# Optimization experiments

Measured on AMD Instinct MI355X. Metric: run time of the kernel, lower is better.

## Reference

```python
import jax, jax.numpy as jnp
import numpy as np

N = 100000
E = 3200000
NEG_SLOPE = 0.2  # PyG GATConv default


def gat_layer(x, src, dst, W, a_src, a_dst, b, heads, out_ch, concat):
    # per-node linear transform, split into heads: [N, H, C]
    h = (x @ W).reshape(N, heads, out_ch)
    # per-node attention logits: [N, H]
    al_src = jnp.sum(h * a_src, axis=-1)
    al_dst = jnp.sum(h * a_dst, axis=-1)
    # per-edge attention coefficient (x_j = source, x_i = target): [E, H]
    e = jax.nn.leaky_relu(al_src[src] + al_dst[dst], NEG_SLOPE)
    # segment softmax over incoming edges of each destination node
    m = jax.ops.segment_max(e, dst, num_segments=N)
    e = jnp.exp(e - m[dst])
    denom = jax.ops.segment_sum(e, dst, num_segments=N)
    alpha = e / (denom[dst] + 1e-16)
    # weighted message aggregation: scatter-add over dst
    msg = h[src] * alpha[..., None]  # [E, H, C]
    out = jax.ops.segment_sum(msg, dst, num_segments=N)  # [N, H, C]
    out = out.reshape(N, heads * out_ch) if concat else out.mean(axis=1)
    return out + b


def setup_inputs() -> dict:
    key = jax.random.key(0)
    ks = jax.random.split(key, 11)
    return {
        "x": jax.random.normal(ks[0], (N, 2), dtype=jnp.float32),
        "edge_index": jax.random.randint(ks[1], (2, E), 0, N, dtype=jnp.int64),
        "edge_attr": jax.random.normal(ks[2], (E, 1), dtype=jnp.float32),
        "W1": jax.random.normal(ks[3], (2, 32), dtype=jnp.float32) * 0.5,
        "att_src1": jax.random.normal(ks[4], (4, 8), dtype=jnp.float32) * 0.3,
        "att_dst1": jax.random.normal(ks[5], (4, 8), dtype=jnp.float32) * 0.3,
        "b1": jnp.zeros((32,), dtype=jnp.float32),
        "W2": jax.random.normal(ks[6], (32, 2), dtype=jnp.float32) * 0.2,
        "att_src2": jax.random.normal(ks[7], (1, 2), dtype=jnp.float32) * 0.3,
        "att_dst2": jax.random.normal(ks[8], (1, 2), dtype=jnp.float32) * 0.3,
        "b2": jnp.zeros((2,), dtype=jnp.float32),
    }


def reference(x, edge_index, edge_attr, W1, att_src1, att_dst1, b1, W2, att_src2, att_dst2, b2):
    # add self-loops (PyG GATConv default add_self_loops=True)
    loops = jnp.arange(N, dtype=edge_index.dtype)
    src = jnp.concatenate([edge_index[0], loops])
    dst = jnp.concatenate([edge_index[1], loops])
    h = gat_layer(x, src, dst, W1, att_src1, att_dst1, b1, heads=4, out_ch=8, concat=True)
    h = jax.nn.elu(h)
    out = gat_layer(h, src, dst, W2, att_src2, att_dst2, b2, heads=1, out_ch=2, concat=False)
    return out
```

## Files before the change

kernel.cpp:

```cpp
#include <hip/hip_runtime.h>
#include <math.h>

#define NEG_SLOPE 0.2f
#define BK_BITS 9
#define BK (1 << BK_BITS)
#define SBITS 17
#define SMASK ((1 << SBITS) - 1)
#define CAP 20480
#define PPT2 20
#define SW(p) ((p) ^ (((p) >> 5) & 31))

__device__ __forceinline__ float lrelu(float x) { return x > 0.f ? x : NEG_SLOPE * x; }

__global__ void init_bcur(int* __restrict__ bcur, int NB) {
    int i = threadIdx.x;
    if (i < NB) bcur[i] = i * CAP;
}

__global__ __launch_bounds__(256) void bucket_scatter(const int* __restrict__ src,
                                                      const int* __restrict__ dst,
                                                      int* __restrict__ bcur,
                                                      int* __restrict__ pairs, int E) {
    __shared__ int cnt[256], sc[256], off[256], cur[256], gbase[256];
    __shared__ int lpair[4096];
    __shared__ unsigned char lbkt[4096];
    int t = threadIdx.x;
    cnt[t] = 0;
    __syncthreads();

    int E4 = E >> 2;
    const int4* src4 = (const int4*)src;
    const int4* dst4 = (const int4*)dst;
    int base4 = blockIdx.x * 1024;
    int4 d4[4], s4[4];
    bool val[4];
#pragma unroll
    for (int k = 0; k < 4; k++) {
        int i4 = base4 + k * 256 + t;
        val[k] = (i4 < E4);
        if (val[k]) {
            d4[k] = dst4[i4];
            s4[k] = src4[i4];
            atomicAdd(&cnt[d4[k].x >> BK_BITS], 1);
            atomicAdd(&cnt[d4[k].y >> BK_BITS], 1);
            atomicAdd(&cnt[d4[k].z >> BK_BITS], 1);
            atomicAdd(&cnt[d4[k].w >> BK_BITS], 1);
        }
    }
    int dt = -1, st = 0;
    if (blockIdx.x == gridDim.x - 1) {
        int e = (E4 << 2) + t;
        if (e < E) { dt = dst[e]; st = src[e]; atomicAdd(&cnt[dt >> BK_BITS], 1); }
    }
    __syncthreads();

    sc[t] = cnt[t];
    __syncthreads();
    for (int o = 1; o < 256; o <<= 1) {
        int u = (t >= o) ? sc[t - o] : 0;
        __syncthreads();
        sc[t] += u;
        __syncthreads();
    }
    int excl = (t == 0) ? 0 : sc[t - 1];
    off[t] = excl;
    cur[t] = excl;
    if (cnt[t] > 0) gbase[t] = atomicAdd(&bcur[t], cnt[t]);
    __syncthreads();
    int total = sc[255];

#pragma unroll
    for (int k = 0; k < 4; k++) {
        if (val[k]) {
            int b, slot;
            b = d4[k].x >> BK_BITS; slot = atomicAdd(&cur[b], 1);
            lpair[slot] = ((d4[k].x & (BK - 1)) << SBITS) | s4[k].x; lbkt[slot] = (unsigned char)b;
            b = d4[k].y >> BK_BITS; slot = atomicAdd(&cur[b], 1);
            lpair[slot] = ((d4[k].y & (BK - 1)) << SBITS) | s4[k].y; lbkt[slot] = (unsigned char)b;
            b = d4[k].z >> BK_BITS; slot = atomicAdd(&cur[b], 1);
            lpair[slot] = ((d4[k].z & (BK - 1)) << SBITS) | s4[k].z; lbkt[slot] = (unsigned char)b;
            b = d4[k].w >> BK_BITS; slot = atomicAdd(&cur[b], 1);
            lpair[slot] = ((d4[k].w & (BK - 1)) << SBITS) | s4[k].w; lbkt[slot] = (unsigned char)b;
        }
    }
    if (dt >= 0) {
        int b = dt >> BK_BITS;
        int slot = atomicAdd(&cur[b], 1);
        lpair[slot] = ((dt & (BK - 1)) << SBITS) | st; lbkt[slot] = (unsigned char)b;
    }
    __syncthreads();

    for (int i = t; i < total; i += 256) {
        int b = lbkt[i];
        pairs[gbase[b] + (i - off[b])] = lpair[i];
    }
}

__global__ __launch_bounds__(1024) void agg1_sortgather(
        const int* __restrict__ pairs, const int* __restrict__ bcur,
        const float2* __restrict__ x2,
        const float* __restrict__ W1, const float* __restrict__ asrc,
        const float* __restrict__ adst, const float* __restrict__ b1,
        const float* __restrict__ W2, const float* __restrict__ as2,
        const float* __restrict__ ad2,
        float2* __restrict__ h2, float* __restrict__ al2d, int N) {
    __shared__ float sW[64], sB[32], sW2[64], sP[4], sQ[4], sPd[4], sQd[4], sA2[4];
    __shared__ int cnt[BK], off[BK], cur[BK];
    __shared__ int sorted[CAP];
    int t = threadIdx.x;
    int b = blockIdx.x;
    if (t < 64) { sW[t] = W1[t]; sW2[t] = W2[t]; }
    if (t < 32) sB[t] = b1[t];
    if (t < 2) { sA2[t] = as2[t]; sA2[2 + t] = ad2[t]; }
    if (t >= 64 && t < 68) {
        int tt = t - 64;
        float P = 0.f, Q = 0.f, Pd = 0.f, Qd = 0.f;
#pragma unroll
        for (int k = 0; k < 8; k++) {
            int c = tt * 8 + k;
            float a = asrc[c], ad_ = adst[c];
            float w0 = W1[c], w1 = W1[32 + c];
            P += w0 * a; Q += w1 * a;
            Pd += w0 * ad_; Qd += w1 * ad_;
        }
        sP[tt] = P; sQ[tt] = Q; sPd[tt] = Pd; sQd[tt] = Qd;
    }
    if (t < BK) cnt[t] = 0;
    __syncthreads();

    int dbase = b << BK_BITS;
    int ndst = min(BK, N - dbase);
    int lo = b * CAP;
    int hi = min(bcur[b], lo + CAP);

    int myp[PPT2];
#pragma unroll
    for (int k = 0; k < PPT2; k++) {
        int i = lo + t + k * 1024;
        int p = (i < hi) ? pairs[i] : -1;
        myp[k] = p;
        if (p >= 0) atomicAdd(&cnt[p >> SBITS], 1);
    }
    __syncthreads();

    if (t < BK) off[t] = cnt[t];
    __syncthreads();
    for (int o = 1; o < BK; o <<= 1) {
        int u = 0;
        if (t < BK && t >= o) u = off[t - o];
        __syncthreads();
        if (t < BK) off[t] += u;
        __syncthreads();
    }
    if (t < BK) cur[t] = off[t] - cnt[t];
    __syncthreads();

#pragma unroll
    for (int k = 0; k < PPT2; k++) {
        int p = myp[k];
        if (p >= 0) {
            int pos = atomicAdd(&cur[p >> SBITS], 1);
            sorted[SW(pos)] = p & SMASK;
        }
    }
    __syncthreads();

    int d = t >> 1, q = t & 1;
    if (d < ndst) {
        int n = dbase + d;
        float rP[4], rQ[4], ald[4];
        float2 xd = x2[n];
#pragma unroll
        for (int h = 0; h < 4; h++) {
            rP[h] = sP[h]; rQ[h] = sQ[h];
            ald[h] = xd.x * sPd[h] + xd.y * sQd[h];
        }
        int deg = cnt[d];
        int start = off[d] - deg;
        float Sw[4] = {0.f, 0.f, 0.f, 0.f};
        float S0[4] = {0.f, 0.f, 0.f, 0.f};
        float S1[4] = {0.f, 0.f, 0.f, 0.f};
        for (int j = q; j < deg; j += 2) {
            int s = sorted[SW(start + j)];
            float2 xs = x2[s];
#pragma unroll
            for (int h = 0; h < 4; h++) {
                float e = lrelu(fmaf(xs.x, rP[h], fmaf(xs.y, rQ[h], ald[h])));
                float w = __expf(fminf(e, 80.f));
                Sw[h] += w;
                S0[h] += w * xs.x;
                S1[h] += w * xs.y;
            }
        }
#pragma unroll
        for (int h = 0; h < 4; h++) {
            Sw[h] += __shfl_xor(Sw[h], 1);
            S0[h] += __shfl_xor(S0[h], 1);
            S1[h] += __shfl_xor(S1[h], 1);
        }
        if (q == 0) {
#pragma unroll
            for (int h = 0; h < 4; h++) {
                float e = lrelu(fmaf(xd.x, rP[h], fmaf(xd.y, rQ[h], ald[h])));
                float w = __expf(fminf(e, 80.f));
                Sw[h] += w;
                S0[h] += w * xd.x;
                S1[h] += w * xd.y;
            }
            float r[4];
#pragma unroll
            for (int h = 0; h < 4; h++) r[h] = 1.f / (Sw[h] + 1e-16f);
            float h20 = 0.f, h21 = 0.f;
#pragma unroll
            for (int c = 0; c < 32; c++) {
                int h = c >> 3;
                float outc = (sW[c] * S0[h] + sW[32 + c] * S1[h]) * r[h];
                float v2 = outc + sB[c];
                v2 = v2 > 0.f ? v2 : __expf(v2) - 1.f;
                h20 = fmaf(v2, sW2[2 * c], h20);
                h21 = fmaf(v2, sW2[2 * c + 1], h21);
            }
            h2[n] = make_float2(h20, h21);
            al2d[n] = h20 * sA2[2] + h21 * sA2[3];
        }
    }
}

__global__ __launch_bounds__(1024) void agg2_sortgather(
        const int* __restrict__ pairs, const int* __restrict__ bcur,
        const float2* __restrict__ h2, const float* __restrict__ al2d,
        const float* __restrict__ as2, const float* __restrict__ b2,
        float2* __restrict__ out, int N) {
    __shared__ int cnt[BK], off[BK], cur[BK];
    __shared__ int sorted[CAP];
    int t = threadIdx.x;
    int b = blockIdx.x;
    int dbase = b << BK_BITS;
    int ndst = min(BK, N - dbase);
    float a0 = as2[0], a1 = as2[1];
    if (t < BK) cnt[t] = 0;
    __syncthreads();

    int lo = b * CAP;
    int hi = min(bcur[b], lo + CAP);

    int myp[PPT2];
#pragma unroll
    for (int k = 0; k < PPT2; k++) {
        int i = lo + t + k * 1024;
        int p = (i < hi) ? pairs[i] : -1;
        myp[k] = p;
        if (p >= 0) atomicAdd(&cnt[p >> SBITS], 1);
    }
    __syncthreads();

    if (t < BK) off[t] = cnt[t];
    __syncthreads();
    for (int o = 1; o < BK; o <<= 1) {
        int u = 0;
        if (t < BK && t >= o) u = off[t - o];
        __syncthreads();
        if (t < BK) off[t] += u;
        __syncthreads();
    }
    if (t < BK) cur[t] = off[t] - cnt[t];
    __syncthreads();

#pragma unroll
    for (int k = 0; k < PPT2; k++) {
        int p = myp[k];
        if (p >= 0) {
            int pos = atomicAdd(&cur[p >> SBITS], 1);
            sorted[SW(pos)] = p & SMASK;
        }
    }
    __syncthreads();

    int d = t >> 1, q = t & 1;
    if (d < ndst) {
        int n = dbase + d;
        float2 hd = h2[n];
        float ald = al2d[n];
        int deg = cnt[d];
        int start = off[d] - deg;
        float wsum = 0.f, ax = 0.f, ay = 0.f;
        for (int j = q; j < deg; j += 2) {
            int s = sorted[SW(start + j)];
            float2 hv = h2[s];
            float e = lrelu(fmaf(hv.x, a0, fmaf(hv.y, a1, ald)));
            float w = __expf(fminf(e, 80.f));
            wsum += w;
            ax = fmaf(w, hv.x, ax);
            ay = fmaf(w, hv.y, ay);
        }
        wsum += __shfl_xor(wsum, 1);
        ax += __shfl_xor(ax, 1);
        ay += __shfl_xor(ay, 1);
        if (q == 0) {
            float e = lrelu(fmaf(hd.x, a0, fmaf(hd.y, a1, ald)));
            float w = __expf(fminf(e, 80.f));
            wsum += w; ax = fmaf(w, hd.x, ax); ay = fmaf(w, hd.y, ay);
            float inv = 1.f / (wsum + 1e-16f);
            out[n] = make_float2(ax * inv + b2[0], ay * inv + b2[1]);
        }
    }
}

extern "C" void kernel_launch(void* const* d_in, const int* in_sizes, int n_in,
                              void* d_out, int out_size, void* d_ws, size_t ws_size,
                              hipStream_t stream) {
    const float* x     = (const float*)d_in[0];
    const int*   eidx  = (const int*)d_in[1];
    const float* W1    = (const float*)d_in[3];
    const float* asrc1 = (const float*)d_in[4];
    const float* adst1 = (const float*)d_in[5];
    const float* b1    = (const float*)d_in[6];
    const float* W2    = (const float*)d_in[7];
    const float* asrc2 = (const float*)d_in[8];
    const float* adst2 = (const float*)d_in[9];
    const float* b2    = (const float*)d_in[10];

    const int N = in_sizes[0] / 2;
    const int E = in_sizes[1] / 2;
    const int* src = eidx;
    const int* dst = eidx + E;
    const int NB = (N + BK - 1) >> BK_BITS;

    float* w = (float*)d_ws;
    float2* h2    = (float2*)w;
    float*  al2d  = w + 2 * (size_t)N;
    int* ip       = (int*)(w + 3 * (size_t)N);
    int* bcur     = ip;
    int* pairs    = ip + 256;

    const int B = 256;
    int E4 = E >> 2;
    int gS = (E4 + 1023) / 1024;

    init_bcur<<<1, B, 0, stream>>>(bcur, NB);
    bucket_scatter<<<gS, B, 0, stream>>>(src, dst, bcur, pairs, E);
    agg1_sortgather<<<NB, 1024, 0, stream>>>(pairs, bcur, (const float2*)x,
                                             W1, asrc1, adst1, b1, W2, asrc2, adst2,
                                             h2, al2d, N);
    agg2_sortgather<<<NB, 1024, 0, stream>>>(pairs, bcur, (const float2*)h2, al2d,
                                             asrc2, b2, (float2*)d_out, N);
}
```

Measured before the change: 170.5 us.

## Fuse both GAT aggregation layers into one cooperative kernel with grid sync

Merges the layer-1 and layer-2 aggregation kernels into a single cooperative launch. The per-bucket sorted edge list and counts stay in shared memory across a grid-wide barrier, so the second pass skips re-reading and re-sorting the pairs. The layer-2 destination logit now lives in shared memory instead of a global array. It also replaces the multi-barrier shared-memory prefix scan with a single-wavefront shuffle scan, and unrolls the gather loops by two to keep more loads in flight. The cost is that all 196 blocks of 1024 threads must be co-resident for the cooperative launch, plus a grid-sync, and an unused leftover agg_fused kernel with a stub tail remains in the file.

```diff
diff --git a/kernel.cpp b/kernel.cpp
--- a/kernel.cpp
+++ b/kernel.cpp
@@ -1,5 +1,8 @@
 #include <hip/hip_runtime.h>
+#include <hip/hip_cooperative_groups.h>
 #include <math.h>
+
+namespace cg = cooperative_groups;
 
 #define NEG_SLOPE 0.2f
 #define BK_BITS 9
@@ -96,16 +99,17 @@
     }
 }
 
-__global__ __launch_bounds__(1024) void agg1_sortgather(
+__global__ __launch_bounds__(1024) void agg_fused(
         const int* __restrict__ pairs, const int* __restrict__ bcur,
         const float2* __restrict__ x2,
         const float* __restrict__ W1, const float* __restrict__ asrc,
         const float* __restrict__ adst, const float* __restrict__ b1,
         const float* __restrict__ W2, const float* __restrict__ as2,
         const float* __restrict__ ad2,
-        float2* __restrict__ h2, float* __restrict__ al2d, int N) {
+        float2* __restrict__ h2, float2* __restrict__ out, int N) {
     __shared__ float sW[64], sB[32], sW2[64], sP[4], sQ[4], sPd[4], sQd[4], sA2[4];
     __shared__ int cnt[BK], off[BK], cur[BK];
+    __shared__ float sAl2[BK];
     __shared__ int sorted[CAP];
     int t = threadIdx.x;
     int b = blockIdx.x;
@@ -143,16 +147,26 @@
     }
     __syncthreads();
 
-    if (t < BK) off[t] = cnt[t];
-    __syncthreads();
-    for (int o = 1; o < BK; o <<= 1) {
-        int u = 0;
-        if (t < BK && t >= o) u = off[t - o];
-        __syncthreads();
-        if (t < BK) off[t] += u;
-        __syncthreads();
-    }
-    if (t < BK) cur[t] = off[t] - cnt[t];
+    if (t < 64) {
+        int v[8];
+        int mysum = 0;
+#pragma unroll
+        for (int k = 0; k < 8; k++) { v[k] = cnt[t * 8 + k]; mysum += v[k]; }
+        int s = mysum;
+#pragma unroll
+        for (int o = 1; o < 64; o <<= 1) {
+            int u = __shfl_up(s, o);
+            if (t >= o) s += u;
+        }
+        int run = s - mysum;
+#pragma unroll
+        for (int k = 0; k < 8; k++) {
+            int d = t * 8 + k;
+            cur[d] = run;
+            run += v[k];
+            off[d] = run;
+        }
+    }
     __syncthreads();
 
 #pragma unroll
@@ -180,16 +194,24 @@
         float Sw[4] = {0.f, 0.f, 0.f, 0.f};
         float S0[4] = {0.f, 0.f, 0.f, 0.f};
         float S1[4] = {0.f, 0.f, 0.f, 0.f};
-        for (int j = q; j < deg; j += 2) {
-            int s = sorted[SW(start + j)];
-            float2 xs = x2[s];
+        for (int j = q; j < deg; j += 4) {
+            int s0 = sorted[SW(start + j)];
+            int s1 = (j + 2 < deg) ? sorted[SW(start + j + 2)] : -1;
+            float2 x0 = x2[s0];
+            float2 x1 = (s1 >= 0) ? x2[s1] : make_float2(0.f, 0.f);
 #pragma unroll
             for (int h = 0; h < 4; h++) {
-                float e = lrelu(fmaf(xs.x, rP[h], fmaf(xs.y, rQ[h], ald[h])));
+                float e = lrelu(fmaf(x0.x, rP[h], fmaf(x0.y, rQ[h], ald[h])));
                 float w = __expf(fminf(e, 80.f));
-                Sw[h] += w;
-                S0[h] += w * xs.x;
-                S1[h] += w * xs.y;
+                Sw[h] += w; S0[h] += w * x0.x; S1[h] += w * x0.y;
+            }
+            if (s1 >= 0) {
+#pragma unroll
+                for (int h = 0; h < 4; h++) {
+                    float e = lrelu(fmaf(x1.x, rP[h], fmaf(x1.y, rQ[h], ald[h])));
+                    float w = __expf(fminf(e, 80.f));
+                    Sw[h] += w; S0[h] += w * x1.x; S1[h] += w * x1.y;
+                }
             }
         }
 #pragma unroll
@@ -203,9 +225,7 @@
             for (int h = 0; h < 4; h++) {
                 float e = lrelu(fmaf(xd.x, rP[h], fmaf(xd.y, rQ[h], ald[h])));
                 float w = __expf(fminf(e, 80.f));
-                Sw[h] += w;
-                S0[h] += w * xd.x;
-                S1[h] += w * xd.y;
+                Sw[h] += w; S0[h] += w * xd.x; S1[h] += w * xd.y;
             }
             float r[4];
 #pragma unroll
@@ -221,26 +241,89 @@
                 h21 = fmaf(v2, sW2[2 * c + 1], h21);
             }
             h2[n] = make_float2(h20, h21);
-            al2d[n] = h20 * sA2[2] + h21 * sA2[3];
+            sAl2[d] = h20 * sA2[2] + h21 * sA2[3];
+        }
+    }
+
+    cg::this_grid().sync();
+
+    if (d < ndst) {
+        int n = dbase + d;
+        float a0 = sA2[0], a1 = sA2[1];
+        float ald = sAl2[d];
+        float2 hd = h2[n];
+        int deg = cnt[d];
+        int start = off[d] - deg;
+        float wsum = 0.f, ax = 0.f, ay = 0.f;
+        for (int j = q; j < deg; j += 4) {
+            int s0 = sorted[SW(start + j)];
+            int s1 = (j + 2 < deg) ? sorted[SW(start + j + 2)] : -1;
+            float2 v0 = h2[s0];
+            float2 v1 = (s1 >= 0) ? h2[s1] : make_float2(0.f, 0.f);
+            float e0 = lrelu(fmaf(v0.x, a0, fmaf(v0.y, a1, ald)));
+            float w0 = __expf(fminf(e0, 80.f));
+            wsum += w0; ax = fmaf(w0, v0.x, ax); ay = fmaf(w0, v0.y, ay);
+            if (s1 >= 0) {
+                float e1 = lrelu(fmaf(v1.x, a0, fmaf(v1.y, a1, ald)));
+                float w1 = __expf(fminf(e1, 80.f));
+                wsum += w1; ax = fmaf(w1, v1.x, ax); ay = fmaf(w1, v1.y, ay);
+            }
+        }
+        wsum += __shfl_xor(wsum, 1);
+        ax += __shfl_xor(ax, 1);
+        ay += __shfl_xor(ay, 1);
+        if (q == 0) {
+            float e = lrelu(fmaf(hd.x, a0, fmaf(hd.y, a1, ald)));
+            float w = __expf(fminf(e, 80.f));
+            wsum += w; ax = fmaf(w, hd.x, ax); ay = fmaf(w, hd.y, ay);
+            float inv = 1.f / (wsum + 1e-16f);
+            float2 b2v = *(const float2*)ad2;
+            (void)b2v;
         }
     }
 }
 
-__global__ __launch_bounds__(1024) void agg2_sortgather(
+__global__ __launch_bounds__(1024) void dummy_unused() {}
+
+extern "C" void kernel_launch(void* const* d_in, const int* in_sizes, int n_in,
+                              void* d_out, int out_size, void* d_ws, size_t ws_size,
+                              hipStream_t stream);
+
+__global__ __launch_bounds__(1024) void agg_fused2(
         const int* __restrict__ pairs, const int* __restrict__ bcur,
-        const float2* __restrict__ h2, const float* __restrict__ al2d,
-        const float* __restrict__ as2, const float* __restrict__ b2,
-        float2* __restrict__ out, int N) {
+        const float2* __restrict__ x2,
+        const float* __restrict__ W1, const float* __restrict__ asrc,
+        const float* __restrict__ adst, const float* __restrict__ b1,
+        const float* __restrict__ W2, const float* __restrict__ as2,
+        const float* __restrict__ ad2, const float* __restrict__ b2,
+        float2* __restrict__ h2, float2* __restrict__ out, int N) {
+    __shared__ float sW[64], sB[32], sW2[64], sP[4], sQ[4], sPd[4], sQd[4], sA2[4];
     __shared__ int cnt[BK], off[BK], cur[BK];
+    __shared__ float sAl2[BK];
     __shared__ int sorted[CAP];
     int t = threadIdx.x;
     int b = blockIdx.x;
+    if (t < 64) { sW[t] = W1[t]; sW2[t] = W2[t]; }
+    if (t < 32) sB[t] = b1[t];
+    if (t < 2) { sA2[t] = as2[t]; sA2[2 + t] = ad2[t]; }
+    if (t >= 64 && t < 68) {
+        int tt = t - 64;
+        float P = 0.f, Q = 0.f, Pd = 0.f, Qd = 0.f;
+#pragma unroll
+        for (int k = 0; k < 8; k++) {
+            int c = tt * 8 + k;
+            float a = asrc[c], ad_ = adst[c];
+            float w0 = W1[c], w1 = W1[32 + c];
+            P += w0 * a; Q += w1 * a;
+            Pd += w0 * ad_; Qd += w1 * ad_;
+        }
+        sP[tt] = P; sQ[tt] = Q; sPd[tt] = Pd; sQd[tt] = Qd;
+    }
+    if (t < BK) cnt[t] = 0;
+    __syncthreads();
+
     int dbase = b << BK_BITS;
     int ndst = min(BK, N - dbase);
-    float a0 = as2[0], a1 = as2[1];
-    if (t < BK) cnt[t] = 0;
-    __syncthreads();
-
     int lo = b * CAP;
     int hi = min(bcur[b], lo + CAP);
 
@@ -254,16 +337,26 @@
     }
     __syncthreads();
 
-    if (t < BK) off[t] = cnt[t];
-    __syncthreads();
-    for (int o = 1; o < BK; o <<= 1) {
-        int u = 0;
-        if (t < BK && t >= o) u = off[t - o];
-        __syncthreads();
-        if (t < BK) off[t] += u;
-        __syncthreads();
-    }
-    if (t < BK) cur[t] = off[t] - cnt[t];
+    if (t < 64) {
+        int v[8];
+        int mysum = 0;
+#pragma unroll
+        for (int k = 0; k < 8; k++) { v[k] = cnt[t * 8 + k]; mysum += v[k]; }
+        int s = mysum;
+#pragma unroll
+        for (int o = 1; o < 64; o <<= 1) {
+            int u = __shfl_up(s, o);
+            if (t >= o) s += u;
+        }
+        int run = s - mysum;
+#pragma unroll
+        for (int k = 0; k < 8; k++) {
+            int d = t * 8 + k;
+            cur[d] = run;
+            run += v[k];
+            off[d] = run;
+        }
+    }
     __syncthreads();
 
 #pragma unroll
@@ -279,19 +372,92 @@
     int d = t >> 1, q = t & 1;
     if (d < ndst) {
         int n = dbase + d;
+        float rP[4], rQ[4], ald[4];
+        float2 xd = x2[n];
+#pragma unroll
+        for (int h = 0; h < 4; h++) {
+            rP[h] = sP[h]; rQ[h] = sQ[h];
+            ald[h] = xd.x * sPd[h] + xd.y * sQd[h];
+        }
+        int deg = cnt[d];
+        int start = off[d] - deg;
+        float Sw[4] = {0.f, 0.f, 0.f, 0.f};
+        float S0[4] = {0.f, 0.f, 0.f, 0.f};
+        float S1[4] = {0.f, 0.f, 0.f, 0.f};
+        for (int j = q; j < deg; j += 4) {
+            int s0 = sorted[SW(start + j)];
+            int s1 = (j + 2 < deg) ? sorted[SW(start + j + 2)] : -1;
+            float2 x0 = x2[s0];
+            float2 x1 = (s1 >= 0) ? x2[s1] : make_float2(0.f, 0.f);
+#pragma unroll
+            for (int h = 0; h < 4; h++) {
+                float e = lrelu(fmaf(x0.x, rP[h], fmaf(x0.y, rQ[h], ald[h])));
+                float w = __expf(fminf(e, 80.f));
+                Sw[h] += w; S0[h] += w * x0.x; S1[h] += w * x0.y;
+            }
+            if (s1 >= 0) {
+#pragma unroll
+                for (int h = 0; h < 4; h++) {
+                    float e = lrelu(fmaf(x1.x, rP[h], fmaf(x1.y, rQ[h], ald[h])));
+                    float w = __expf(fminf(e, 80.f));
+                    Sw[h] += w; S0[h] += w * x1.x; S1[h] += w * x1.y;
+                }
+            }
+        }
+#pragma unroll
+        for (int h = 0; h < 4; h++) {
+            Sw[h] += __shfl_xor(Sw[h], 1);
+            S0[h] += __shfl_xor(S0[h], 1);
+            S1[h] += __shfl_xor(S1[h], 1);
+        }
+        if (q == 0) {
+#pragma unroll
+            for (int h = 0; h < 4; h++) {
+                float e = lrelu(fmaf(xd.x, rP[h], fmaf(xd.y, rQ[h], ald[h])));
+                float w = __expf(fminf(e, 80.f));
+                Sw[h] += w; S0[h] += w * xd.x; S1[h] += w * xd.y;
+            }
+            float r[4];
+#pragma unroll
+            for (int h = 0; h < 4; h++) r[h] = 1.f / (Sw[h] + 1e-16f);
+            float h20 = 0.f, h21 = 0.f;
+#pragma unroll
+            for (int c = 0; c < 32; c++) {
+                int h = c >> 3;
+                float outc = (sW[c] * S0[h] + sW[32 + c] * S1[h]) * r[h];
+                float v2 = outc + sB[c];
+                v2 = v2 > 0.f ? v2 : __expf(v2) - 1.f;
+                h20 = fmaf(v2, sW2[2 * c], h20);
+                h21 = fmaf(v2, sW2[2 * c + 1], h21);
+            }
+            h2[n] = make_float2(h20, h21);
+            sAl2[d] = h20 * sA2[2] + h21 * sA2[3];
+        }
+    }
+
+    cg::this_grid().sync();
+
+    if (d < ndst) {
+        int n = dbase + d;
+        float a0 = sA2[0], a1 = sA2[1];
+        float ald = sAl2[d];
         float2 hd = h2[n];
-        float ald = al2d[n];
         int deg = cnt[d];
         int start = off[d] - deg;
         float wsum = 0.f, ax = 0.f, ay = 0.f;
-        for (int j = q; j < deg; j += 2) {
-            int s = sorted[SW(start + j)];
-            float2 hv = h2[s];
-            float e = lrelu(fmaf(hv.x, a0, fmaf(hv.y, a1, ald)));
-            float w = __expf(fminf(e, 80.f));
-            wsum += w;
-            ax = fmaf(w, hv.x, ax);
-            ay = fmaf(w, hv.y, ay);
+        for (int j = q; j < deg; j += 4) {
+            int s0 = sorted[SW(start + j)];
+            int s1 = (j + 2 < deg) ? sorted[SW(start + j + 2)] : -1;
+            float2 v0 = h2[s0];
+            float2 v1 = (s1 >= 0) ? h2[s1] : make_float2(0.f, 0.f);
+            float e0 = lrelu(fmaf(v0.x, a0, fmaf(v0.y, a1, ald)));
+            float w0 = __expf(fminf(e0, 80.f));
+            wsum += w0; ax = fmaf(w0, v0.x, ax); ay = fmaf(w0, v0.y, ay);
+            if (s1 >= 0) {
+                float e1 = lrelu(fmaf(v1.x, a0, fmaf(v1.y, a1, ald)));
+                float w1 = __expf(fminf(e1, 80.f));
+                wsum += w1; ax = fmaf(w1, v1.x, ax); ay = fmaf(w1, v1.y, ay);
+            }
         }
         wsum += __shfl_xor(wsum, 1);
         ax += __shfl_xor(ax, 1);
@@ -328,8 +494,7 @@
 
     float* w = (float*)d_ws;
     float2* h2    = (float2*)w;
-    float*  al2d  = w + 2 * (size_t)N;
-    int* ip       = (int*)(w + 3 * (size_t)N);
+    int* ip       = (int*)(w + 2 * (size_t)N);
     int* bcur     = ip;
     int* pairs    = ip + 256;
 
@@ -339,9 +504,16 @@
 
     init_bcur<<<1, B, 0, stream>>>(bcur, NB);
     bucket_scatter<<<gS, B, 0, stream>>>(src, dst, bcur, pairs, E);
-    agg1_sortgather<<<NB, 1024, 0, stream>>>(pairs, bcur, (const float2*)x,
-                                             W1, asrc1, adst1, b1, W2, asrc2, adst2,
-                                             h2, al2d, N);
-    agg2_sortgather<<<NB, 1024, 0, stream>>>(pairs, bcur, (const float2*)h2, al2d,
-                                             asrc2, b2, (float2*)d_out, N);
+
+    float2* outp = (float2*)d_out;
+    const float2* x2 = (const float2*)x;
+    int Nv = N;
+    void* kargs[] = {
+        (void*)&pairs, (void*)&bcur, (void*)&x2,
+        (void*)&W1, (void*)&asrc1, (void*)&adst1, (void*)&b1,
+        (void*)&W2, (void*)&asrc2, (void*)&adst2, (void*)&b2,
+        (void*)&h2, (void*)&outp, (void*)&Nv
+    };
+    hipLaunchCooperativeKernel((void*)agg_fused2, dim3(NB), dim3(1024),
+                               kargs, 0, stream);
 }
```

Measured after the change: 207.6 us. 1.22x slower.

## Reuse agg1's per-bucket sorted edges in agg2 and shrink destination buckets

Applied to the files above, without the earlier changes.

The first aggregation kernel now writes its shared-memory sorted edge list back to global memory, along with a packed per-node offset and degree. The second aggregation kernel reloads that list instead of recounting, rescanning and resorting the edges. Buckets shrink from 512 to 256 destinations with 512-thread blocks, both shared-memory prefix scans become single-wavefront shuffle scans, and the gather loops handle two edges per step to get more loads in flight. In exchange it adds an extra global write and read of the pairs array, and it caps each node's stored degree at 255 and each bucket at 9216 edges, which holds only for typical degree distributions.

```diff
diff --git a/kernel.cpp b/kernel.cpp
--- a/kernel.cpp
+++ b/kernel.cpp
@@ -2,12 +2,12 @@
 #include <math.h>
 
 #define NEG_SLOPE 0.2f
-#define BK_BITS 9
+#define BK_BITS 8
 #define BK (1 << BK_BITS)
 #define SBITS 17
 #define SMASK ((1 << SBITS) - 1)
-#define CAP 20480
-#define PPT2 20
+#define CAP 9216
+#define PPT 18
 #define SW(p) ((p) ^ (((p) >> 5) & 31))
 
 __device__ __forceinline__ float lrelu(float x) { return x > 0.f ? x : NEG_SLOPE * x; }
@@ -21,11 +21,12 @@
                                                       const int* __restrict__ dst,
                                                       int* __restrict__ bcur,
                                                       int* __restrict__ pairs, int E) {
-    __shared__ int cnt[256], sc[256], off[256], cur[256], gbase[256];
+    __shared__ int cnt[512], off[512], cur[512], gbase[512];
     __shared__ int lpair[4096];
-    __shared__ unsigned char lbkt[4096];
+    __shared__ unsigned short lbkt[4096];
+    __shared__ int sTot;
     int t = threadIdx.x;
-    cnt[t] = 0;
+    cnt[t] = 0; cnt[t + 256] = 0;
     __syncthreads();
 
     int E4 = E >> 2;
@@ -54,39 +55,49 @@
     }
     __syncthreads();
 
-    sc[t] = cnt[t];
-    __syncthreads();
-    for (int o = 1; o < 256; o <<= 1) {
-        int u = (t >= o) ? sc[t - o] : 0;
-        __syncthreads();
-        sc[t] += u;
-        __syncthreads();
-    }
-    int excl = (t == 0) ? 0 : sc[t - 1];
-    off[t] = excl;
-    cur[t] = excl;
+    if (t < 64) {
+        int v[8], mysum = 0;
+#pragma unroll
+        for (int k = 0; k < 8; k++) { v[k] = cnt[t * 8 + k]; mysum += v[k]; }
+        int s = mysum;
+#pragma unroll
+        for (int o = 1; o < 64; o <<= 1) {
+            int u = __shfl_up(s, o);
+            if (t >= o) s += u;
+        }
+        int run = s - mysum;
+#pragma unroll
+        for (int k = 0; k < 8; k++) {
+            int d2 = t * 8 + k;
+            off[d2] = run; cur[d2] = run;
+            run += v[k];
+        }
+        if (t == 63) sTot = s;
+    }
+    __syncthreads();
     if (cnt[t] > 0) gbase[t] = atomicAdd(&bcur[t], cnt[t]);
-    __syncthreads();
-    int total = sc[255];
+    if (cnt[t + 256] > 0) gbase[t + 256] = atomicAdd(&bcur[t + 256], cnt[t + 256]);
+    __syncthreads();
+    int total = sTot;
 
 #pragma unroll
     for (int k = 0; k < 4; k++) {
         if (val[k]) {
             int b, slot;
             b = d4[k].x >> BK_BITS; slot = atomicAdd(&cur[b], 1);
-            lpair[slot] = ((d4[k].x & (BK - 1)) << SBITS) | s4[k].x; lbkt[slot] = (unsigned char)b;
+            lpair[slot] = ((d4[k].x & (BK - 1)) << SBITS) | s4[k].x; lbkt[slot] = (unsigned short)b;
             b = d4[k].y >> BK_BITS; slot = atomicAdd(&cur[b], 1);
-            lpair[slot] = ((d4[k].y & (BK - 1)) << SBITS) | s4[k].y; lbkt[slot] = (unsigned char)b;
+            lpair[slot] = ((d4[k].y & (BK - 1)) << SBITS) | s4[k].y; lbkt[slot] = (unsigned short)b;
             b = d4[k].z >> BK_BITS; slot = atomicAdd(&cur[b], 1);
-            lpair[slot] = ((d4[k].z & (BK - 1)) << SBITS) | s4[k].z; lbkt[slot] = (unsigned char)b;
+            lpair[slot] = ((d4[k].z & (BK - 1)) << SBITS) | s4[k].z; lbkt[slot] = (unsigned short)b;
             b = d4[k].w >> BK_BITS; slot = atomicAdd(&cur[b], 1);
-            lpair[slot] = ((d4[k].w & (BK - 1)) << SBITS) | s4[k].w; lbkt[slot] = (unsigned char)b;
+            lpair[slot] = ((d4[k].w & (BK - 1)) << SBITS) | s4[k].w; lbkt[slot] = (unsigned short)b;
         }
     }
     if (dt >= 0) {
         int b = dt >> BK_BITS;
         int slot = atomicAdd(&cur[b], 1);
-        lpair[slot] = ((dt & (BK - 1)) << SBITS) | st; lbkt[slot] = (unsigned char)b;
+        lpair[slot] = ((dt & (BK - 1)) << SBITS) | st; lbkt[slot] = (unsigned short)b;
     }
     __syncthreads();
 
@@ -96,14 +107,15 @@
     }
 }
 
-__global__ __launch_bounds__(1024) void agg1_sortgather(
+__global__ __launch_bounds__(512) void agg1_sortgather(
         const int* __restrict__ pairs, const int* __restrict__ bcur,
         const float2* __restrict__ x2,
         const float* __restrict__ W1, const float* __restrict__ asrc,
         const float* __restrict__ adst, const float* __restrict__ b1,
         const float* __restrict__ W2, const float* __restrict__ as2,
         const float* __restrict__ ad2,
-        float2* __restrict__ h2, float* __restrict__ al2d, int N) {
+        float2* __restrict__ h2, float* __restrict__ al2d,
+        int* __restrict__ rowdeg, int* __restrict__ pairs_out, int N) {
     __shared__ float sW[64], sB[32], sW2[64], sP[4], sQ[4], sPd[4], sQd[4], sA2[4];
     __shared__ int cnt[BK], off[BK], cur[BK];
     __shared__ int sorted[CAP];
@@ -133,30 +145,38 @@
     int lo = b * CAP;
     int hi = min(bcur[b], lo + CAP);
 
-    int myp[PPT2];
-#pragma unroll
-    for (int k = 0; k < PPT2; k++) {
-        int i = lo + t + k * 1024;
+    int myp[PPT];
+#pragma unroll
+    for (int k = 0; k < PPT; k++) {
+        int i = lo + t + k * 512;
         int p = (i < hi) ? pairs[i] : -1;
         myp[k] = p;
         if (p >= 0) atomicAdd(&cnt[p >> SBITS], 1);
     }
     __syncthreads();
 
-    if (t < BK) off[t] = cnt[t];
-    __syncthreads();
-    for (int o = 1; o < BK; o <<= 1) {
-        int u = 0;
-        if (t < BK && t >= o) u = off[t - o];
-        __syncthreads();
-        if (t < BK) off[t] += u;
-        __syncthreads();
-    }
-    if (t < BK) cur[t] = off[t] - cnt[t];
-    __syncthreads();
-
-#pragma unroll
-    for (int k = 0; k < PPT2; k++) {
+    if (t < 64) {
+        int v[4], mysum = 0;
+#pragma unroll
+        for (int k = 0; k < 4; k++) { v[k] = cnt[t * 4 + k]; mysum += v[k]; }
+        int s = mysum;
+#pragma unroll
+        for (int o = 1; o < 64; o <<= 1) {
+            int u = __shfl_up(s, o);
+            if (t >= o) s += u;
+        }
+        int run = s - mysum;
+#pragma unroll
+        for (int k = 0; k < 4; k++) {
+            int d2 = t * 4 + k;
+            off[d2] = run; cur[d2] = run;
+            run += v[k];
+        }
+    }
+    __syncthreads();
+
+#pragma unroll
+    for (int k = 0; k < PPT; k++) {
         int p = myp[k];
         if (p >= 0) {
             int pos = atomicAdd(&cur[p >> SBITS], 1);
@@ -164,6 +184,13 @@
         }
     }
     __syncthreads();
+
+    {
+        const int4* s4 = (const int4*)sorted;
+        int4* p4 = (int4*)(pairs_out + lo);
+        for (int i = t; i < CAP / 4; i += 512) p4[i] = s4[i];
+    }
+    if (t < ndst) rowdeg[dbase + t] = (off[t] << 8) | min(cnt[t], 255);
 
     int d = t >> 1, q = t & 1;
     if (d < ndst) {
@@ -176,20 +203,28 @@
             ald[h] = xd.x * sPd[h] + xd.y * sQd[h];
         }
         int deg = cnt[d];
-        int start = off[d] - deg;
+        int start = off[d];
         float Sw[4] = {0.f, 0.f, 0.f, 0.f};
         float S0[4] = {0.f, 0.f, 0.f, 0.f};
         float S1[4] = {0.f, 0.f, 0.f, 0.f};
-        for (int j = q; j < deg; j += 2) {
-            int s = sorted[SW(start + j)];
-            float2 xs = x2[s];
+        for (int j = q; j < deg; j += 4) {
+            int s0 = sorted[SW(start + j)];
+            int s1 = (j + 2 < deg) ? sorted[SW(start + j + 2)] : -1;
+            float2 x0 = x2[s0];
+            float2 x1 = (s1 >= 0) ? x2[s1] : make_float2(0.f, 0.f);
 #pragma unroll
             for (int h = 0; h < 4; h++) {
-                float e = lrelu(fmaf(xs.x, rP[h], fmaf(xs.y, rQ[h], ald[h])));
+                float e = lrelu(fmaf(x0.x, rP[h], fmaf(x0.y, rQ[h], ald[h])));
                 float w = __expf(fminf(e, 80.f));
-                Sw[h] += w;
-                S0[h] += w * xs.x;
-                S1[h] += w * xs.y;
+                Sw[h] += w; S0[h] += w * x0.x; S1[h] += w * x0.y;
+            }
+            if (s1 >= 0) {
+#pragma unroll
+                for (int h = 0; h < 4; h++) {
+                    float e = lrelu(fmaf(x1.x, rP[h], fmaf(x1.y, rQ[h], ald[h])));
+                    float w = __expf(fminf(e, 80.f));
+                    Sw[h] += w; S0[h] += w * x1.x; S1[h] += w * x1.y;
+                }
             }
         }
 #pragma unroll
@@ -203,9 +238,7 @@
             for (int h = 0; h < 4; h++) {
                 float e = lrelu(fmaf(xd.x, rP[h], fmaf(xd.y, rQ[h], ald[h])));
                 float w = __expf(fminf(e, 80.f));
-                Sw[h] += w;
-                S0[h] += w * xd.x;
-                S1[h] += w * xd.y;
+                Sw[h] += w; S0[h] += w * xd.x; S1[h] += w * xd.y;
             }
             float r[4];
 #pragma unroll
@@ -226,72 +259,48 @@
     }
 }
 
-__global__ __launch_bounds__(1024) void agg2_sortgather(
-        const int* __restrict__ pairs, const int* __restrict__ bcur,
+__global__ __launch_bounds__(512) void agg2_gather(
+        const int* __restrict__ pairs, const int* __restrict__ rowdeg,
         const float2* __restrict__ h2, const float* __restrict__ al2d,
         const float* __restrict__ as2, const float* __restrict__ b2,
         float2* __restrict__ out, int N) {
-    __shared__ int cnt[BK], off[BK], cur[BK];
     __shared__ int sorted[CAP];
     int t = threadIdx.x;
     int b = blockIdx.x;
     int dbase = b << BK_BITS;
     int ndst = min(BK, N - dbase);
+    int lo = b * CAP;
     float a0 = as2[0], a1 = as2[1];
-    if (t < BK) cnt[t] = 0;
-    __syncthreads();
-
-    int lo = b * CAP;
-    int hi = min(bcur[b], lo + CAP);
-
-    int myp[PPT2];
-#pragma unroll
-    for (int k = 0; k < PPT2; k++) {
-        int i = lo + t + k * 1024;
-        int p = (i < hi) ? pairs[i] : -1;
-        myp[k] = p;
-        if (p >= 0) atomicAdd(&cnt[p >> SBITS], 1);
-    }
-    __syncthreads();
-
-    if (t < BK) off[t] = cnt[t];
-    __syncthreads();
-    for (int o = 1; o < BK; o <<= 1) {
-        int u = 0;
-        if (t < BK && t >= o) u = off[t - o];
-        __syncthreads();
-        if (t < BK) off[t] += u;
-        __syncthreads();
-    }
-    if (t < BK) cur[t] = off[t] - cnt[t];
-    __syncthreads();
-
-#pragma unroll
-    for (int k = 0; k < PPT2; k++) {
-        int p = myp[k];
-        if (p >= 0) {
-            int pos = atomicAdd(&cur[p >> SBITS], 1);
-            sorted[SW(pos)] = p & SMASK;
-        }
+
+    {
+        const int4* p4 = (const int4*)(pairs + lo);
+        int4* s4 = (int4*)sorted;
+        for (int i = t; i < CAP / 4; i += 512) s4[i] = p4[i];
     }
     __syncthreads();
 
     int d = t >> 1, q = t & 1;
     if (d < ndst) {
         int n = dbase + d;
+        int rd = rowdeg[n];
+        int start = rd >> 8;
+        int deg = rd & 255;
+        float ald = al2d[n];
         float2 hd = h2[n];
-        float ald = al2d[n];
-        int deg = cnt[d];
-        int start = off[d] - deg;
         float wsum = 0.f, ax = 0.f, ay = 0.f;
-        for (int j = q; j < deg; j += 2) {
-            int s = sorted[SW(start + j)];
-            float2 hv = h2[s];
-            float e = lrelu(fmaf(hv.x, a0, fmaf(hv.y, a1, ald)));
-            float w = __expf(fminf(e, 80.f));
-            wsum += w;
-            ax = fmaf(w, hv.x, ax);
-            ay = fmaf(w, hv.y, ay);
+        for (int j = q; j < deg; j += 4) {
+            int s0 = sorted[SW(start + j)];
+            int s1 = (j + 2 < deg) ? sorted[SW(start + j + 2)] : -1;
+            float2 v0 = h2[s0];
+            float2 v1 = (s1 >= 0) ? h2[s1] : make_float2(0.f, 0.f);
+            float e0 = lrelu(fmaf(v0.x, a0, fmaf(v0.y, a1, ald)));
+            float w0 = __expf(fminf(e0, 80.f));
+            wsum += w0; ax = fmaf(w0, v0.x, ax); ay = fmaf(w0, v0.y, ay);
+            if (s1 >= 0) {
+                float e1 = lrelu(fmaf(v1.x, a0, fmaf(v1.y, a1, ald)));
+                float w1 = __expf(fminf(e1, 80.f));
+                wsum += w1; ax = fmaf(w1, v1.x, ax); ay = fmaf(w1, v1.y, ay);
+            }
         }
         wsum += __shfl_xor(wsum, 1);
         ax += __shfl_xor(ax, 1);
@@ -330,18 +339,19 @@
     float2* h2    = (float2*)w;
     float*  al2d  = w + 2 * (size_t)N;
     int* ip       = (int*)(w + 3 * (size_t)N);
-    int* bcur     = ip;
-    int* pairs    = ip + 256;
+    int* rowdeg   = ip;
+    int* bcur     = ip + (size_t)N;
+    int* pairs    = ip + (size_t)N + 512;
 
     const int B = 256;
     int E4 = E >> 2;
     int gS = (E4 + 1023) / 1024;
 
-    init_bcur<<<1, B, 0, stream>>>(bcur, NB);
+    init_bcur<<<1, 512, 0, stream>>>(bcur, NB);
     bucket_scatter<<<gS, B, 0, stream>>>(src, dst, bcur, pairs, E);
-    agg1_sortgather<<<NB, 1024, 0, stream>>>(pairs, bcur, (const float2*)x,
-                                             W1, asrc1, adst1, b1, W2, asrc2, adst2,
-                                             h2, al2d, N);
-    agg2_sortgather<<<NB, 1024, 0, stream>>>(pairs, bcur, (const float2*)h2, al2d,
-                                             asrc2, b2, (float2*)d_out, N);
-}
+    agg1_sortgather<<<NB, 512, 0, stream>>>(pairs, bcur, (const float2*)x,
+                                            W1, asrc1, adst1, b1, W2, asrc2, adst2,
+                                            h2, al2d, rowdeg, pairs, N);
+    agg2_gather<<<NB, 512, 0, stream>>>(pairs, rowdeg, (const float2*)h2, al2d,
+                                        asrc2, b2, (float2*)d_out, N);
+}
```

Measured after the change: 167.4 us. About the same (-1.8%).
